# Optimization experiments

Hardware: AMD Instinct MI355X
Metric: run time of the kernel (lower is better)

Reference implementation:

```python
import jax, jax.numpy as jnp
import numpy as np

B, T, D = 32, 2048, 512
BATCH_SIZE = 32  # config.batch_size: number of MVN draws


def setup_inputs() -> dict:
    key = jax.random.key(0)
    k1, k2 = jax.random.split(key)
    x = jax.random.normal(k1, (B, T, D), dtype=jnp.float32)
    z = jax.random.normal(k2, (BATCH_SIZE, D), dtype=jnp.float32)  # standard-normal noise for reparameterized MVN draw
    return {"x": x, "z": z}


def reference(x, z):
    # mean over batch and time -> [D]
    mean = jnp.mean(x, axis=(0, 1))
    # per-batch covariance over time axis, then mean over batch -> [D, D]
    t = x.shape[1]
    xc = x - jnp.mean(x, axis=1, keepdims=True)
    # sum over b and t fused: equals mean_b( xc_b^T xc_b / (t-1) )
    cov = jnp.einsum('btd,bte->de', xc, xc) / ((t - 1) * x.shape[0])
    # multivariate normal draw via Cholesky reparameterization:
    # sample = mean + z @ L^T, L L^T = cov
    L = jnp.linalg.cholesky(cov)
    return mean + z @ L.T
```

## Files before the change

kernel.cpp:

```cpp
#include <hip/hip_runtime.h>

#define Dn 512
#define Bn 32
#define Tn 2048
#define BT 65536

typedef unsigned short u16;
typedef __attribute__((ext_vector_type(8))) short short8;
typedef __attribute__((ext_vector_type(4))) float floatx4;

__device__ __forceinline__ u16 f2bf(float f) {
    unsigned u = __float_as_uint(f);
    unsigned r = (u + 0x7FFFu + ((u >> 16) & 1u)) >> 16;
    return (u16)r;
}
__device__ __forceinline__ float bf2f(u16 s) { return __uint_as_float(((unsigned)s) << 16); }

#define REP64(X) X(0) X(1) X(2) X(3) X(4) X(5) X(6) X(7) X(8) X(9) X(10) X(11) X(12) X(13) X(14) X(15) \
    X(16) X(17) X(18) X(19) X(20) X(21) X(22) X(23) X(24) X(25) X(26) X(27) X(28) X(29) X(30) X(31) \
    X(32) X(33) X(34) X(35) X(36) X(37) X(38) X(39) X(40) X(41) X(42) X(43) X(44) X(45) X(46) X(47) \
    X(48) X(49) X(50) X(51) X(52) X(53) X(54) X(55) X(56) X(57) X(58) X(59) X(60) X(61) X(62) X(63)
#define REPJ(OP, K) OP(K,0) OP(K,1) OP(K,2) OP(K,3) OP(K,4) OP(K,5) OP(K,6) OP(K,7) OP(K,8) OP(K,9) \
    OP(K,10) OP(K,11) OP(K,12) OP(K,13) OP(K,14) OP(K,15) OP(K,16) OP(K,17) OP(K,18) OP(K,19) \
    OP(K,20) OP(K,21) OP(K,22) OP(K,23) OP(K,24) OP(K,25) OP(K,26) OP(K,27) OP(K,28) OP(K,29) \
    OP(K,30) OP(K,31) OP(K,32) OP(K,33) OP(K,34) OP(K,35) OP(K,36) OP(K,37) OP(K,38) OP(K,39) \
    OP(K,40) OP(K,41) OP(K,42) OP(K,43) OP(K,44) OP(K,45) OP(K,46) OP(K,47) OP(K,48) OP(K,49) \
    OP(K,50) OP(K,51) OP(K,52) OP(K,53) OP(K,54) OP(K,55) OP(K,56) OP(K,57) OP(K,58) OP(K,59) \
    OP(K,60) OP(K,61) OP(K,62) OP(K,63)
#define REPQ(OP, C) OP(C,0,0,0) OP(C,1,0,1) OP(C,2,0,2) OP(C,3,0,3) OP(C,4,1,0) OP(C,5,1,1) OP(C,6,1,2) OP(C,7,1,3) \
    OP(C,8,2,0) OP(C,9,2,1) OP(C,10,2,2) OP(C,11,2,3) OP(C,12,3,0) OP(C,13,3,1) OP(C,14,3,2) OP(C,15,3,3) \
    OP(C,16,4,0) OP(C,17,4,1) OP(C,18,4,2) OP(C,19,4,3) OP(C,20,5,0) OP(C,21,5,1) OP(C,22,5,2) OP(C,23,5,3) \
    OP(C,24,6,0) OP(C,25,6,1) OP(C,26,6,2) OP(C,27,6,3) OP(C,28,7,0) OP(C,29,7,1) OP(C,30,7,2) OP(C,31,7,3) \
    OP(C,32,8,0) OP(C,33,8,1) OP(C,34,8,2) OP(C,35,8,3) OP(C,36,9,0) OP(C,37,9,1) OP(C,38,9,2) OP(C,39,9,3) \
    OP(C,40,10,0) OP(C,41,10,1) OP(C,42,10,2) OP(C,43,10,3) OP(C,44,11,0) OP(C,45,11,1) OP(C,46,11,2) OP(C,47,11,3) \
    OP(C,48,12,0) OP(C,49,12,1) OP(C,50,12,2) OP(C,51,12,3) OP(C,52,13,0) OP(C,53,13,1) OP(C,54,13,2) OP(C,55,13,3) \
    OP(C,56,14,0) OP(C,57,14,1) OP(C,58,14,2) OP(C,59,14,3) OP(C,60,15,0) OP(C,61,15,1) OP(C,62,15,2) OP(C,63,15,3)
#define REPW(OP) OP(0,0,1,2,3) OP(1,4,5,6,7) OP(2,8,9,10,11) OP(3,12,13,14,15) OP(4,16,17,18,19) \
    OP(5,20,21,22,23) OP(6,24,25,26,27) OP(7,28,29,30,31) OP(8,32,33,34,35) OP(9,36,37,38,39) \
    OP(10,40,41,42,43) OP(11,44,45,46,47) OP(12,48,49,50,51) OP(13,52,53,54,55) OP(14,56,57,58,59) \
    OP(15,60,61,62,63)
#define REP16C(OP, C) OP(C,0) OP(C,1) OP(C,2) OP(C,3) OP(C,4) OP(C,5) OP(C,6) OP(C,7) \
    OP(C,8) OP(C,9) OP(C,10) OP(C,11) OP(C,12) OP(C,13) OP(C,14) OP(C,15)

__global__ __launch_bounds__(256) void k_transpose(const float* __restrict__ x,
                                                   u16* __restrict__ Xt) {
    int tt = blockIdx.x;
    int dt = blockIdx.y;
    int b  = blockIdx.z;
    __shared__ u16 sT[64][68];
    int tid = threadIdx.x;
    int row = tid >> 4;
    int c4  = (tid & 15) * 4;
    const float* src = x + ((long)b * Tn + (long)tt * 64) * Dn + dt * 64;
#pragma unroll
    for (int q = 0; q < 4; q++) {
        int r = row + q * 16;
        floatx4 v = *(const floatx4*)(src + (long)r * Dn + c4);
        sT[c4 + 0][r] = f2bf(v[0]);
        sT[c4 + 1][r] = f2bf(v[1]);
        sT[c4 + 2][r] = f2bf(v[2]);
        sT[c4 + 3][r] = f2bf(v[3]);
    }
    __syncthreads();
    int drow = tid >> 3;
    int koff = (tid & 7) * 8;
    long kout = (long)b * Tn + (long)tt * 64 + koff;
#pragma unroll
    for (int p = 0; p < 2; p++) {
        int dr = drow + p * 32;
        u16 tmp[8];
#pragma unroll
        for (int j = 0; j < 8; j++) tmp[j] = sT[dr][koff + j];
        *(short8*)(Xt + (long)(dt * 64 + dr) * BT + kout) = *(short8*)tmp;
    }
}

__global__ __launch_bounds__(256) void k_mu(const u16* __restrict__ Xt,
                                            float* __restrict__ mu) {
    int tid = threadIdx.x;
    int wave = tid >> 6, lane = tid & 63;
    int p = blockIdx.x * 4 + wave;
    int b = p >> 9, d = p & 511;
    const u16* src = Xt + (long)d * BT + (long)b * Tn;
    float s = 0.f;
#pragma unroll
    for (int c = 0; c < 4; c++) {
        short8 v = *(const short8*)(src + c * 512 + lane * 8);
#pragma unroll
        for (int j = 0; j < 8; j++) s += bf2f((u16)v[j]);
    }
#pragma unroll
    for (int off = 32; off; off >>= 1) s += __shfl_down(s, off, 64);
    if (lane == 0) mu[p] = s * (1.0f / Tn);
}

#define LDK 40
__global__ __launch_bounds__(256) void k_gram(const u16* __restrict__ Xt,
                                              float* __restrict__ partial) {
    int chunk = blockIdx.x;
    int pos = blockIdx.y;
    int di = (pos < 4) ? 0 : (pos < 7) ? 1 : (pos < 9) ? 2 : 3;
    int start = di * 4 - (di * (di - 1)) / 2;
    int ei = di + (pos - start);
    int d0 = di * 128, e0 = ei * 128;

    __shared__ u16 sA[128 * LDK];
    __shared__ u16 sB[128 * LDK];
    int tid = threadIdx.x;
    int wave = tid >> 6, lane = tid & 63;
    int wm = wave & 1, wn = wave >> 1;
    int lrow = tid >> 2;
    int lk = (tid & 3) * 8;
    const u16* gA = Xt + (long)(d0 + lrow) * BT + (long)chunk * 4096 + lk;
    const u16* gB = Xt + (long)(e0 + lrow) * BT + (long)chunk * 4096 + lk;
    int m = lane & 15, g = lane >> 4;

    floatx4 acc[4][4] = {};
    for (int kk = 0; kk < 4096; kk += 32) {
        short8 a0 = *(const short8*)(gA + kk);
        short8 a1 = *(const short8*)(gA + 64l * BT + kk);
        short8 b0 = *(const short8*)(gB + kk);
        short8 b1 = *(const short8*)(gB + 64l * BT + kk);
        __syncthreads();
        *(short8*)(sA + lrow * LDK + lk) = a0;
        *(short8*)(sA + (lrow + 64) * LDK + lk) = a1;
        *(short8*)(sB + lrow * LDK + lk) = b0;
        *(short8*)(sB + (lrow + 64) * LDK + lk) = b1;
        __syncthreads();
        short8 af[4], bf[4];
#pragma unroll
        for (int i = 0; i < 4; i++)
            af[i] = *(const short8*)(sA + (wm * 64 + i * 16 + m) * LDK + g * 8);
#pragma unroll
        for (int j = 0; j < 4; j++)
            bf[j] = *(const short8*)(sB + (wn * 64 + j * 16 + m) * LDK + g * 8);
#pragma unroll
        for (int i = 0; i < 4; i++)
#pragma unroll
            for (int j = 0; j < 4; j++)
                acc[i][j] = __builtin_amdgcn_mfma_f32_16x16x32_bf16(af[i], bf[j], acc[i][j], 0, 0, 0);
    }
    float* P = partial + (long)chunk * (512l * 512);
    int col = lane & 15, rowg = (lane >> 4) * 4;
#pragma unroll
    for (int i = 0; i < 4; i++)
#pragma unroll
        for (int j = 0; j < 4; j++) {
            int rr = d0 + wm * 64 + i * 16 + rowg;
            int cc = e0 + wn * 64 + j * 16 + col;
#pragma unroll
            for (int r = 0; r < 4; r++) P[(long)(rr + r) * 512 + cc] = acc[i][j][r];
        }
}

__global__ __launch_bounds__(256) void k_assemble(const float* __restrict__ partial,
                                                  const float* __restrict__ mu,
                                                  float* __restrict__ A) {
    int d = blockIdx.y;
    int e = blockIdx.x * 256 + threadIdx.x;
    int bd = d >> 7, be = e >> 7;
    long idx = (bd <= be) ? ((long)d * 512 + e) : ((long)e * 512 + d);
    float s = 0.f;
#pragma unroll
    for (int c = 0; c < 16; c++) s += partial[c * (512l * 512) + idx];
    float msum = 0.f;
#pragma unroll
    for (int b = 0; b < 32; b++) msum += mu[b * 512 + d] * mu[b * 512 + e];
    A[(long)d * 512 + e] = (s - (float)Tn * msum) * (1.0f / ((Tn - 1.0f) * Bn));
}

__global__ __launch_bounds__(64, 1) void k_chol_panel(float* __restrict__ A, int kb) {
    const int k0 = kb * 64;
    const int lane = threadIdx.x;
    __shared__ float sD[64 * 68];
    __shared__ float sInv[64];
    const floatx4 z4 = {0.f, 0.f, 0.f, 0.f};

    const float* Dr = A + (long)(k0 + lane) * 512 + k0;
#define LDV(Q,A0,A1,A2,A3) floatx4 v##Q = *(const floatx4*)(Dr + 4*(Q));
    REPW(LDV)
#undef LDV
#define DECR(C,M,Mq,e) float r##M = v##Mq[(e)];
    REPQ(DECR, 0)
#undef DECR

    float vinv = 0.f;
#define SH1(K,J) float t##J = ((J) > (K)) ? __shfl(lik, (J), 64) : 0.0f;
#define FM1(K,J) if ((J) > (K)) r##J = fmaf(-lik, t##J, r##J);
#define STEP(K) { float akk = __shfl(r##K, (K), 64); float sd = sqrtf(akk); \
                  float inv = 1.0f / sd; float lik = (lane == (K)) ? sd : r##K * inv; \
                  r##K = lik; if (lane == (K)) vinv = inv; REPJ(SH1, K) REPJ(FM1, K) }
    REP64(STEP)
#undef STEP
#undef FM1
#undef SH1

    if (blockIdx.x == 0) {
        float* W = A + (long)(k0 + lane) * 512 + k0;
#define STW(Q,A0,A1,A2,A3) { floatx4 w; w[0]=r##A0; w[1]=r##A1; w[2]=r##A2; w[3]=r##A3; \
                             *(floatx4*)(W + 4*(Q)) = w; }
        REPW(STW)
#undef STW
        return;
    }

#define STD(Q,A0,A1,A2,A3) { floatx4 w; w[0]=r##A0; w[1]=r##A1; w[2]=r##A2; w[3]=r##A3; \
                             *(floatx4*)(sD + lane * 68 + 4*(Q)) = w; }
    REPW(STD)
#undef STD
    sInv[lane] = vinv;
    __syncthreads();

    int rbase = k0 + 64 + (blockIdx.x - 1) * 64;
    const float* R = A + (long)(rbase + lane) * 512 + k0;
#define LDA(Q,A0,A1,A2,A3) floatx4 u##Q = *(const floatx4*)(R + 4*(Q));
    REPW(LDA)
#undef LDA
#define DECA(C,M,Mq,e) float a##M = u##Mq[(e)];
    REPQ(DECA, 0)
#undef DECA
#define LQ(C,Q) floatx4 q##Q = ((C) > 4*(Q)) ? *(const floatx4*)(sD + (C) * 68 + 4*(Q)) : z4;
#define TF(C,M,Mq,e) if ((M) < (C)) acc##e = fmaf(a##M, q##Mq[(e)], acc##e);
#define TSTEP(C) { REP16C(LQ, C) float acc0 = 0.f, acc1 = 0.f, acc2 = 0.f, acc3 = 0.f; \
                   REPQ(TF, C) a##C = (a##C - ((acc0 + acc1) + (acc2 + acc3))) * sInv[(C)]; }
    REP64(TSTEP)
#undef TSTEP
#undef TF
#undef LQ

    float* Wr = A + (long)(rbase + lane) * 512 + k0;
#define STA(Q,A0,A1,A2,A3) { floatx4 w; w[0]=a##A0; w[1]=a##A1; w[2]=a##A2; w[3]=a##A3; \
                             *(floatx4*)(Wr + 4*(Q)) = w; }
    REPW(STA)
#undef STA
}

__global__ __launch_bounds__(256) void k_chol_update(float* __restrict__ A, int kb) {
    int k0 = kb * 64, base = k0 + 64;
    int idx = blockIdx.x, ti = 0;
    while (idx > ti) { idx -= ti + 1; ti++; }
    int tj = idx;
    int r0 = base + ti * 64, c0 = base + tj * 64;
    __shared__ float sI[64][65];
    __shared__ float sJ[64][65];
    int tid = threadIdx.x;
    int row = tid >> 4, c4 = (tid & 15) * 4;
#pragma unroll
    for (int q = 0; q < 4; q++) {
        int rr = row + q * 16;
        *(floatx4*)&sI[rr][c4] = *(const floatx4*)(A + (long)(r0 + rr) * 512 + k0 + c4);
        *(floatx4*)&sJ[rr][c4] = *(const floatx4*)(A + (long)(c0 + rr) * 512 + k0 + c4);
    }
    __syncthreads();
    int ri = (tid >> 4) * 4, cj = (tid & 15) * 4;
    float acc[4][4] = {};
    for (int k = 0; k < 64; k += 4) {
        floatx4 av[4], bv[4];
#pragma unroll
        for (int ii = 0; ii < 4; ii++) av[ii] = *(const floatx4*)&sI[ri + ii][k];
#pragma unroll
        for (int jj = 0; jj < 4; jj++) bv[jj] = *(const floatx4*)&sJ[cj + jj][k];
#pragma unroll
        for (int ii = 0; ii < 4; ii++)
#pragma unroll
            for (int jj = 0; jj < 4; jj++)
#pragma unroll
                for (int q = 0; q < 4; q++)
                    acc[ii][jj] = fmaf(av[ii][q], bv[jj][q], acc[ii][jj]);
    }
#pragma unroll
    for (int ii = 0; ii < 4; ii++) {
        float* dst = A + (long)(r0 + ri + ii) * 512 + c0 + cj;
        floatx4 old = *(const floatx4*)dst;
#pragma unroll
        for (int jj = 0; jj < 4; jj++) old[jj] -= acc[ii][jj];
        *(floatx4*)dst = old;
    }
}

__global__ __launch_bounds__(512) void k_output(const float* __restrict__ z,
                                                const float* __restrict__ A,
                                                const float* __restrict__ mu,
                                                float* __restrict__ out) {
    int i = blockIdx.x, d = threadIdx.x;
    __shared__ float sz[512];
    sz[d] = z[(long)i * 512 + d];
    __syncthreads();
    float mean = 0.f;
#pragma unroll
    for (int b = 0; b < 32; b++) mean += mu[b * 512 + d];
    mean *= (1.0f / 32.0f);
    const float* Lr = A + (long)d * 512;
    float acc = 0.f;
    int dmax = d + 1;
    int e4 = dmax & ~3;
    for (int e = 0; e < e4; e += 4) {
        floatx4 l = *(const floatx4*)(Lr + e);
        acc += l[0] * sz[e] + l[1] * sz[e + 1] + l[2] * sz[e + 2] + l[3] * sz[e + 3];
    }
    for (int e = e4; e < dmax; e++) acc += Lr[e] * sz[e];
    out[(long)i * 512 + d] = mean + acc;
}

extern "C" void kernel_launch(void* const* d_in, const int* in_sizes, int n_in,
                              void* d_out, int out_size, void* d_ws, size_t ws_size,
                              hipStream_t stream) {
    const float* x = (const float*)d_in[0];
    const float* z = (const float*)d_in[1];
    float* out = (float*)d_out;
    char* ws = (char*)d_ws;
    u16* Xt = (u16*)ws;
    float* mu = (float*)(ws + 67108864);
    float* partial = (float*)(ws + 67108864 + 65536);
    float* A = (float*)(ws + 67108864 + 65536 + 16777216);

    k_transpose<<<dim3(32, 8, 32), 256, 0, stream>>>(x, Xt);
    k_mu<<<4096, 256, 0, stream>>>(Xt, mu);
    k_gram<<<dim3(16, 10), 256, 0, stream>>>(Xt, partial);
    k_assemble<<<dim3(2, 512), 256, 0, stream>>>(partial, mu, A);
    for (int kb = 0; kb < 8; kb++) {
        int nb = 7 - kb;
        k_chol_panel<<<nb + 1, 64, 0, stream>>>(A, kb);
        int tiles = nb * (nb + 1) / 2;
        if (tiles > 0) k_chol_update<<<tiles, 256, 0, stream>>>(A, kb);
    }
    k_output<<<32, 512, 0, stream>>>(z, A, mu, out);
}
```

Measured before the change: 672.4 us.

## Fuse mean into transpose, split Gram over more chunks, load via LDS DMA

The per-(batch,feature) sums are now accumulated with atomics inside the transpose kernel, which removes the separate k_mu pass over Xt. The Gram kernel splits K into 64 chunks instead of 16, so 640 blocks are launched instead of 160, and it fills shared memory with global_load_lds direct loads instead of staging through registers. The tradeoff is four times more partial-sum traffic for k_assemble to read and a larger workspace. Unpadded LDS rows may also cause bank conflicts.

Result: no change. 665.0 us (-1.1%).

```diff
diff --git a/kernel.cpp b/kernel.cpp
--- a/kernel.cpp
+++ b/kernel.cpp
@@ -4,6 +4,8 @@
 #define Bn 32
 #define Tn 2048
 #define BT 65536
+#define NCHUNK 64
+#define CHUNK_K 1024
 
 typedef unsigned short u16;
 typedef __attribute__((ext_vector_type(8))) short short8;
@@ -15,6 +17,10 @@
     return (u16)r;
 }
 __device__ __forceinline__ float bf2f(u16 s) { return __uint_as_float(((unsigned)s) << 16); }
+
+#define GLL(gp, sp) __builtin_amdgcn_global_load_lds( \
+    (const __attribute__((address_space(1))) void*)(gp), \
+    (__attribute__((address_space(3))) void*)(sp), 16, 0, 0)
 
 #define REP64(X) X(0) X(1) X(2) X(3) X(4) X(5) X(6) X(7) X(8) X(9) X(10) X(11) X(12) X(13) X(14) X(15) \
     X(16) X(17) X(18) X(19) X(20) X(21) X(22) X(23) X(24) X(25) X(26) X(27) X(28) X(29) X(30) X(31) \
@@ -42,8 +48,14 @@
 #define REP16C(OP, C) OP(C,0) OP(C,1) OP(C,2) OP(C,3) OP(C,4) OP(C,5) OP(C,6) OP(C,7) \
     OP(C,8) OP(C,9) OP(C,10) OP(C,11) OP(C,12) OP(C,13) OP(C,14) OP(C,15)
 
+__global__ __launch_bounds__(256) void k_zero(float* __restrict__ mu) {
+    floatx4 z = {0.f, 0.f, 0.f, 0.f};
+    ((floatx4*)mu)[blockIdx.x * 256 + threadIdx.x] = z;
+}
+
 __global__ __launch_bounds__(256) void k_transpose(const float* __restrict__ x,
-                                                   u16* __restrict__ Xt) {
+                                                   u16* __restrict__ Xt,
+                                                   float* __restrict__ mu) {
     int tt = blockIdx.x;
     int dt = blockIdx.y;
     int b  = blockIdx.z;
@@ -69,34 +81,22 @@
     for (int p = 0; p < 2; p++) {
         int dr = drow + p * 32;
         u16 tmp[8];
-#pragma unroll
-        for (int j = 0; j < 8; j++) tmp[j] = sT[dr][koff + j];
+        float s = 0.f;
+#pragma unroll
+        for (int j = 0; j < 8; j++) {
+            tmp[j] = sT[dr][koff + j];
+            s += bf2f(tmp[j]);
+        }
         *(short8*)(Xt + (long)(dt * 64 + dr) * BT + kout) = *(short8*)tmp;
-    }
-}
-
-__global__ __launch_bounds__(256) void k_mu(const u16* __restrict__ Xt,
-                                            float* __restrict__ mu) {
-    int tid = threadIdx.x;
-    int wave = tid >> 6, lane = tid & 63;
-    int p = blockIdx.x * 4 + wave;
-    int b = p >> 9, d = p & 511;
-    const u16* src = Xt + (long)d * BT + (long)b * Tn;
-    float s = 0.f;
-#pragma unroll
-    for (int c = 0; c < 4; c++) {
-        short8 v = *(const short8*)(src + c * 512 + lane * 8);
-#pragma unroll
-        for (int j = 0; j < 8; j++) s += bf2f((u16)v[j]);
-    }
-#pragma unroll
-    for (int off = 32; off; off >>= 1) s += __shfl_down(s, off, 64);
-    if (lane == 0) mu[p] = s * (1.0f / Tn);
-}
-
-#define LDK 40
-__global__ __launch_bounds__(256) void k_gram(const u16* __restrict__ Xt,
-                                              float* __restrict__ partial) {
+        s += __shfl_down(s, 4, 64);
+        s += __shfl_down(s, 2, 64);
+        s += __shfl_down(s, 1, 64);
+        if ((tid & 7) == 0) atomicAdd(mu + b * 512 + dt * 64 + dr, s);
+    }
+}
+
+__global__ __launch_bounds__(256, 3) void k_gram(const u16* __restrict__ Xt,
+                                                 float* __restrict__ partial) {
     int chunk = blockIdx.x;
     int pos = blockIdx.y;
     int di = (pos < 4) ? 0 : (pos < 7) ? 1 : (pos < 9) ? 2 : 3;
@@ -104,44 +104,47 @@
     int ei = di + (pos - start);
     int d0 = di * 128, e0 = ei * 128;
 
-    __shared__ u16 sA[128 * LDK];
-    __shared__ u16 sB[128 * LDK];
+    __shared__ u16 sA[128 * 32];
+    __shared__ u16 sB[128 * 32];
     int tid = threadIdx.x;
-    int wave = tid >> 6, lane = tid & 63;
-    int wm = wave & 1, wn = wave >> 1;
-    int lrow = tid >> 2;
-    int lk = (tid & 3) * 8;
-    const u16* gA = Xt + (long)(d0 + lrow) * BT + (long)chunk * 4096 + lk;
-    const u16* gB = Xt + (long)(e0 + lrow) * BT + (long)chunk * 4096 + lk;
-    int m = lane & 15, g = lane >> 4;
+    int w = tid >> 6, l = tid & 63;
+    int wm = w & 1, wn = w >> 1;
+    long kbase = (long)chunk * CHUNK_K;
+    int srow = w * 16 + (l >> 2);
+    int sk = (l & 3) * 8;
+    const u16* gA0 = Xt + (long)(d0 + srow) * BT + kbase + sk;
+    const u16* gA1 = gA0 + 64l * BT;
+    const u16* gB0 = Xt + (long)(e0 + srow) * BT + kbase + sk;
+    const u16* gB1 = gB0 + 64l * BT;
+    u16* sA0 = sA + (w * 16) * 32;
+    u16* sA1 = sA0 + 64 * 32;
+    u16* sB0 = sB + (w * 16) * 32;
+    u16* sB1 = sB0 + 64 * 32;
+    int m = l & 15, g = l >> 4;
+    const u16* fA = sA + (wm * 64 + m) * 32 + g * 8;
+    const u16* fB = sB + (wn * 64 + m) * 32 + g * 8;
 
     floatx4 acc[4][4] = {};
-    for (int kk = 0; kk < 4096; kk += 32) {
-        short8 a0 = *(const short8*)(gA + kk);
-        short8 a1 = *(const short8*)(gA + 64l * BT + kk);
-        short8 b0 = *(const short8*)(gB + kk);
-        short8 b1 = *(const short8*)(gB + 64l * BT + kk);
+    for (int kk = 0; kk < CHUNK_K; kk += 32) {
+        GLL(gA0 + kk, sA0);
+        GLL(gA1 + kk, sA1);
+        GLL(gB0 + kk, sB0);
+        GLL(gB1 + kk, sB1);
         __syncthreads();
-        *(short8*)(sA + lrow * LDK + lk) = a0;
-        *(short8*)(sA + (lrow + 64) * LDK + lk) = a1;
-        *(short8*)(sB + lrow * LDK + lk) = b0;
-        *(short8*)(sB + (lrow + 64) * LDK + lk) = b1;
+        short8 af[4], bfv[4];
+#pragma unroll
+        for (int i = 0; i < 4; i++) af[i] = *(const short8*)(fA + i * 16 * 32);
+#pragma unroll
+        for (int j = 0; j < 4; j++) bfv[j] = *(const short8*)(fB + j * 16 * 32);
+#pragma unroll
+        for (int i = 0; i < 4; i++)
+#pragma unroll
+            for (int j = 0; j < 4; j++)
+                acc[i][j] = __builtin_amdgcn_mfma_f32_16x16x32_bf16(af[i], bfv[j], acc[i][j], 0, 0, 0);
         __syncthreads();
-        short8 af[4], bf[4];
-#pragma unroll
-        for (int i = 0; i < 4; i++)
-            af[i] = *(const short8*)(sA + (wm * 64 + i * 16 + m) * LDK + g * 8);
-#pragma unroll
-        for (int j = 0; j < 4; j++)
-            bf[j] = *(const short8*)(sB + (wn * 64 + j * 16 + m) * LDK + g * 8);
-#pragma unroll
-        for (int i = 0; i < 4; i++)
-#pragma unroll
-            for (int j = 0; j < 4; j++)
-                acc[i][j] = __builtin_amdgcn_mfma_f32_16x16x32_bf16(af[i], bf[j], acc[i][j], 0, 0, 0);
     }
     float* P = partial + (long)chunk * (512l * 512);
-    int col = lane & 15, rowg = (lane >> 4) * 4;
+    int col = l & 15, rowg = (l >> 4) * 4;
 #pragma unroll
     for (int i = 0; i < 4; i++)
 #pragma unroll
@@ -162,11 +165,11 @@
     long idx = (bd <= be) ? ((long)d * 512 + e) : ((long)e * 512 + d);
     float s = 0.f;
 #pragma unroll
-    for (int c = 0; c < 16; c++) s += partial[c * (512l * 512) + idx];
+    for (int c = 0; c < NCHUNK; c++) s += partial[c * (512l * 512) + idx];
     float msum = 0.f;
 #pragma unroll
     for (int b = 0; b < 32; b++) msum += mu[b * 512 + d] * mu[b * 512 + e];
-    A[(long)d * 512 + e] = (s - (float)Tn * msum) * (1.0f / ((Tn - 1.0f) * Bn));
+    A[(long)d * 512 + e] = (s - msum * (1.0f / Tn)) * (1.0f / ((Tn - 1.0f) * Bn));
 }
 
 __global__ __launch_bounds__(64, 1) void k_chol_panel(float* __restrict__ A, int kb) {
@@ -289,7 +292,7 @@
     float mean = 0.f;
 #pragma unroll
     for (int b = 0; b < 32; b++) mean += mu[b * 512 + d];
-    mean *= (1.0f / 32.0f);
+    mean *= (1.0f / (32.0f * 2048.0f));
     const float* Lr = A + (long)d * 512;
     float acc = 0.f;
     int dmax = d + 1;
@@ -312,11 +315,11 @@
     u16* Xt = (u16*)ws;
     float* mu = (float*)(ws + 67108864);
     float* partial = (float*)(ws + 67108864 + 65536);
-    float* A = (float*)(ws + 67108864 + 65536 + 16777216);
-
-    k_transpose<<<dim3(32, 8, 32), 256, 0, stream>>>(x, Xt);
-    k_mu<<<4096, 256, 0, stream>>>(Xt, mu);
-    k_gram<<<dim3(16, 10), 256, 0, stream>>>(Xt, partial);
+    float* A = (float*)(ws + 67108864 + 65536 + 67108864);
+
+    k_zero<<<16, 256, 0, stream>>>(mu);
+    k_transpose<<<dim3(32, 8, 32), 256, 0, stream>>>(x, Xt, mu);
+    k_gram<<<dim3(NCHUNK, 10), 256, 0, stream>>>(Xt, partial);
     k_assemble<<<dim3(2, 512), 256, 0, stream>>>(partial, mu, A);
     for (int kb = 0; kb < 8; kb++) {
         int nb = 7 - kb;
```
